# Optimization experiments

Hardware: AMD Instinct MI355X
Metric: run time of the kernel (lower is better)

## Reference

```python
import jax, jax.numpy as jnp
import numpy as np

N_VARS = 200000
M_CONS = 100000
NNZ = 1600000
HID = 128
NEG_SLOPE = 0.01  # torch F.leaky_relu default


def setup_inputs() -> dict:
    key = jax.random.key(0)
    ks = jax.random.split(key, 14)
    s = 0.05
    return {
        "primal": jax.random.normal(ks[0], (N_VARS, HID), jnp.float32),
        "last_primal": jax.random.normal(ks[1], (N_VARS, HID), jnp.float32),
        "dual": jax.random.normal(ks[2], (M_CONS, HID), jnp.float32),
        "rows": jax.random.randint(ks[3], (NNZ,), 0, M_CONS),
        "cols": jax.random.randint(ks[4], (NNZ,), 0, N_VARS),
        "vals": jax.random.normal(ks[5], (NNZ,), jnp.float32),
        "right_hand_side": jax.random.normal(ks[6], (M_CONS, HID), jnp.float32),
        "W1": jax.random.normal(ks[7], (HID, HID), jnp.float32) * s,
        "b1": jax.random.normal(ks[8], (HID,), jnp.float32) * s,
        "W2": jax.random.normal(ks[9], (HID, HID), jnp.float32) * s,
        "b2": jax.random.normal(ks[10], (HID,), jnp.float32) * s,
        "W3": jax.random.normal(ks[11], (HID, HID), jnp.float32) * s,
        "b3": jax.random.normal(ks[12], (HID,), jnp.float32) * s,
        "sigma": jnp.asarray(2.0, jnp.float32),
    }


def reference(primal, last_primal, dual, rows, cols, vals, right_hand_side,
              W1, b1, W2, b2, W3, b3, sigma):
    # X = Theta2(primal) - Theta3(last_primal): [n_vars, hid]
    X = (primal @ W2.T + b2) - (last_primal @ W3.T + b3)
    # sparse.mm(A_coo, X): gather source rows, scale by nnz vals, scatter-add to constraint rows
    msgs = vals[:, None] * X[cols]                      # [nnz, hid]
    AX = jax.ops.segment_sum(msgs, rows, num_segments=M_CONS)  # [m_cons, hid]
    pre = (dual @ W1.T + b1) + sigma * (AX - right_hand_side)
    return jnp.where(pre >= 0, pre, NEG_SLOPE * pre)
```

## Files before the change

kernel.cpp:

```cpp
#include <hip/hip_runtime.h>

#define HID 128
#define NEG_SLOPE 0.01f
#define NB 256
#define CHUNK 2048
#define MAX_RB 512
#define CAP 8192

typedef __attribute__((ext_vector_type(8))) short short8;
typedef __attribute__((ext_vector_type(4))) float f32x4;
typedef __attribute__((ext_vector_type(4))) unsigned u32x4;

__device__ inline unsigned short f2bfu(float f) {
    unsigned u = __float_as_uint(f);
    u += 0x7fff + ((u >> 16) & 1);
    return (unsigned short)(u >> 16);
}
__device__ inline float bf2f_lo(unsigned x) { return __uint_as_float((x & 0xffffu) << 16); }
__device__ inline float bf2f_hi(unsigned x) { return __uint_as_float(x & 0xffff0000u); }

__device__ inline unsigned cvtpk(float lo, float hi) {
    unsigned r;
    asm("v_cvt_pk_bf16_f32 %0, %1, %2" : "=v"(r) : "v"(lo), "v"(hi));
    return r;
}

#define MFMA_SW(accv, wfrag, xfrag) \
    asm("v_mfma_f32_16x16x32_bf16 %0, %1, %2, %0" : "+v"(accv) : "v"(wfrag), "v"(xfrag))

__global__ __launch_bounds__(256) void k_prep(
    const float* __restrict__ W1, const float* __restrict__ W2, const float* __restrict__ W3,
    unsigned short* __restrict__ Wcat, short8* __restrict__ W1F)
{
    int gid = blockIdx.x * 256 + threadIdx.x;
    if (gid < 128 * 256) {
        int n = gid >> 8, k = gid & 255;
        float v = (k < 128) ? W2[n * 128 + k] : -W3[n * 128 + (k - 128)];
        Wcat[gid] = f2bfu(v);
    } else if (gid < 128 * 256 + 2048) {
        int e = gid - 128 * 256;
        int lane = e & 63, ks = (e >> 6) & 3, nb = e >> 8;
        int row = nb * 16 + (lane & 15);
        int k0 = ks * 32 + ((lane >> 4) << 3);
        short8 v;
        #pragma unroll
        for (int j = 0; j < 8; ++j)
            v[j] = (short)f2bfu(W1[row * 128 + k0 + j]);
        W1F[e] = v;
    }
}

__device__ inline void load_a(const float* __restrict__ Ap, long rowbase, int nrows_tot,
                              int rrow, int rcol, float4 (&araw)[2][8])
{
    const float4 z4 = {0.f, 0.f, 0.f, 0.f};
    #pragma unroll
    for (int rg = 0; rg < 2; ++rg) {
        long row = rowbase + rrow + rg * 16;
        const float4* rp = (const float4*)(Ap + row * HID + rcol);
        if (row < nrows_tot) {
            #pragma unroll
            for (int ks = 0; ks < 4; ++ks) {
                araw[rg][ks * 2 + 0] = rp[ks * 8 + 0];
                araw[rg][ks * 2 + 1] = rp[ks * 8 + 1];
            }
        } else {
            #pragma unroll
            for (int u = 0; u < 8; ++u) araw[rg][u] = z4;
        }
    }
}

__device__ inline void conv_a(const float4 (&araw)[2][8], u32x4 (&af)[2][4])
{
    #pragma unroll
    for (int rg = 0; rg < 2; ++rg)
        #pragma unroll
        for (int ks = 0; ks < 4; ++ks) {
            float4 x0 = araw[rg][ks * 2 + 0], x1 = araw[rg][ks * 2 + 1];
            af[rg][ks][0] = cvtpk(x0.x, x0.y);
            af[rg][ks][1] = cvtpk(x0.z, x0.w);
            af[rg][ks][2] = cvtpk(x1.x, x1.y);
            af[rg][ks][3] = cvtpk(x1.z, x1.w);
        }
}

__device__ inline void mfma_half(f32x4 (&acc)[2][8], const u32x4 (&af)[2][4],
                                 const short8* Blds, int base, int l)
{
    #pragma unroll
    for (int ks = 0; ks < 4; ++ks)
        #pragma unroll
        for (int nb = 0; nb < 8; ++nb) {
            short8 bv = Blds[base + (nb * 4 + ks) * 64 + l];
            MFMA_SW(acc[0][nb], bv, af[0][ks]);
            MFMA_SW(acc[1][nb], bv, af[1][ks]);
        }
}

__global__ __launch_bounds__(256, 2) void k_theta_bfill(
    const float* __restrict__ primal, const float* __restrict__ lastp,
    const short8* __restrict__ Wcat,
    const float* __restrict__ b2, const float* __restrict__ b3,
    unsigned short* __restrict__ Xb, int nvars, int ntiles, int tgrid,
    const int* __restrict__ rows, const int* __restrict__ cols, const float* __restrict__ vals,
    int* __restrict__ cursor, int2* __restrict__ tmp_rc, float* __restrict__ tmp_v, int nnz, int rb,
    const float* __restrict__ dual, const short8* __restrict__ W1F,
    const float* __restrict__ b1, const float* __restrict__ rhs,
    const float* __restrict__ sigp, float* __restrict__ predual, int mcons, int nchunks)
{
    __shared__ short8 Blds[4096];
    const int t = threadIdx.x;

    if (blockIdx.x < (unsigned)tgrid) {
        const int l = t & 63, wv = t >> 6;
        const int rrow = wv * 32 + (l & 15);
        const int rcol = (l >> 4) << 3;
        const int colb = (l >> 4) << 2;

        float4 araw[2][8];
        const long tile0 = blockIdx.x;
        load_a(primal, tile0 * 128, nvars, rrow, rcol, araw);

        #pragma unroll
        for (int i = 0; i < 16; ++i) {
            int e = t + i * 256;
            int lane = e & 63, ks = (e >> 6) & 3, nb = (e >> 8) & 7, hf = e >> 11;
            int row = nb * 16 + (lane & 15);
            int col8 = (hf * 128 + ks * 32 + ((lane >> 4) << 3)) >> 3;
            Blds[e] = Wcat[row * 32 + col8];
        }

        float4 bias[8];
        #pragma unroll
        for (int nb = 0; nb < 8; ++nb) {
            int col = nb * 16 + colb;
            float4 p = *(const float4*)&b2[col];
            float4 q = *(const float4*)&b3[col];
            bias[nb] = make_float4(p.x - q.x, p.y - q.y, p.z - q.z, p.w - q.w);
        }

        __syncthreads();

        const f32x4 z = {0.f, 0.f, 0.f, 0.f};
        f32x4 acc[2][8];
        #pragma unroll
        for (int rg = 0; rg < 2; ++rg)
            #pragma unroll
            for (int nb = 0; nb < 8; ++nb) acc[rg][nb] = z;

        u32x4 af[2][4];

        #pragma unroll 1
        for (long tile = tile0; tile < ntiles; tile += tgrid) {
            conv_a(araw, af);
            load_a(lastp, tile * 128, nvars, rrow, rcol, araw);
            mfma_half(acc, af, Blds, 0, l);

            conv_a(araw, af);
            long nt = tile + tgrid;
            if (nt < ntiles) load_a(primal, nt * 128, nvars, rrow, rcol, araw);
            mfma_half(acc, af, Blds, 2048, l);

            asm volatile("s_nop 7\ns_nop 7");
            #pragma unroll
            for (int rg = 0; rg < 2; ++rg) {
                long row = tile * 128 + rrow + rg * 16;
                if (row < nvars) {
                    #pragma unroll
                    for (int nb = 0; nb < 8; ++nb) {
                        uint2 w;
                        w.x = cvtpk(acc[rg][nb][0] + bias[nb].x, acc[rg][nb][1] + bias[nb].y);
                        w.y = cvtpk(acc[rg][nb][2] + bias[nb].z, acc[rg][nb][3] + bias[nb].w);
                        *(uint2*)&Xb[row * HID + nb * 16 + colb] = w;
                    }
                }
                #pragma unroll
                for (int nb = 0; nb < 8; ++nb) acc[rg][nb] = z;
            }
        }
    } else if (blockIdx.x < (unsigned)(tgrid + nchunks)) {
        int* hist  = (int*)Blds;
        int* basep = hist + NB;
        int cb = blockIdx.x - tgrid;
        long cbase = (long)cb * CHUNK;
        hist[t] = 0;
        __syncthreads();

        int r[8], c[8], b[8], loc[8];
        float v[8];
        #pragma unroll
        for (int i = 0; i < 8; ++i) {
            long e = cbase + i * 256 + t;
            int locv = -1; int bi = 0; int ri = 0, ci = 0; float vi = 0.f;
            if (e < nnz) {
                ri = rows[e]; ci = cols[e]; vi = vals[e];
                bi = ri / rb;
                locv = atomicAdd(&hist[bi], 1);
            }
            r[i] = ri; c[i] = ci; v[i] = vi; b[i] = bi; loc[i] = locv;
        }
        __syncthreads();
        if (hist[t] > 0) basep[t] = atomicAdd(&cursor[t], hist[t]);
        __syncthreads();
        #pragma unroll
        for (int i = 0; i < 8; ++i) {
            if (loc[i] >= 0) {
                int o = basep[b[i]] + loc[i];
                if (o < CAP) {
                    long slot = (long)b[i] * CAP + o;
                    tmp_rc[slot] = make_int2(r[i], c[i]);
                    tmp_v[slot]  = v[i];
                }
            }
        }
    } else {
        const int l = t & 63, wv = t >> 6;
        const int rrow = wv * 32 + (l & 15);
        const int rcol = (l >> 4) << 3;
        const int colb = (l >> 4) << 2;
        const float sigma = *sigp;
        const long rowbase = (long)(blockIdx.x - tgrid - nchunks) * 128;

        float4 araw[2][8];
        load_a(dual, rowbase, mcons, rrow, rcol, araw);

        u32x4 af[2][4];
        conv_a(araw, af);

        const f32x4 z = {0.f, 0.f, 0.f, 0.f};
        f32x4 acc[2][8];
        #pragma unroll
        for (int rg = 0; rg < 2; ++rg)
            #pragma unroll
            for (int nb = 0; nb < 8; ++nb) acc[rg][nb] = z;

        #pragma unroll
        for (int ks = 0; ks < 4; ++ks)
            #pragma unroll
            for (int nb = 0; nb < 8; ++nb) {
                short8 bv = W1F[(nb * 4 + ks) * 64 + l];
                MFMA_SW(acc[0][nb], bv, af[0][ks]);
                MFMA_SW(acc[1][nb], bv, af[1][ks]);
            }
        asm volatile("s_nop 7\ns_nop 7");

        float4 bias[8];
        #pragma unroll
        for (int nb = 0; nb < 8; ++nb)
            bias[nb] = *(const float4*)&b1[nb * 16 + colb];

        #pragma unroll
        for (int rg = 0; rg < 2; ++rg) {
            long row = rowbase + rrow + rg * 16;
            if (row < mcons) {
                #pragma unroll
                for (int nb = 0; nb < 8; ++nb) {
                    long idx = row * HID + nb * 16 + colb;
                    float4 r4 = *(const float4*)&rhs[idx];
                    float4 pre;
                    pre.x = acc[rg][nb][0] + bias[nb].x - sigma * r4.x;
                    pre.y = acc[rg][nb][1] + bias[nb].y - sigma * r4.y;
                    pre.z = acc[rg][nb][2] + bias[nb].z - sigma * r4.z;
                    pre.w = acc[rg][nb][3] + bias[nb].w - sigma * r4.w;
                    *(float4*)&predual[idx] = pre;
                }
            }
        }
    }
}

__global__ __launch_bounds__(256) void k_csr(
    const int2* __restrict__ tmp_rc, const float* __restrict__ tmp_v,
    const int* __restrict__ bucket_fill,
    int* __restrict__ rowstart, int* __restrict__ count, int2* __restrict__ pairs,
    int m, int rb)
{
    __shared__ int cnt[MAX_RB];
    __shared__ int cur[MAX_RB];
    int b = blockIdx.x, t = threadIdx.x;
    int row0 = b * rb;
    int nrows = m - row0; if (nrows > rb) nrows = rb;
    if (nrows <= 0) return;

    for (int i = t; i < nrows; i += 256) cnt[i] = 0;
    __syncthreads();

    long e0 = (long)b * CAP;
    int fill = bucket_fill[b]; if (fill > CAP) fill = CAP;
    long e1 = e0 + fill;
    for (long e = e0 + t; e < e1; e += 256)
        atomicAdd(&cnt[tmp_rc[e].x - row0], 1);
    __syncthreads();

    if (t == 0) {
        int run = (int)e0;
        for (int i = 0; i < nrows; ++i) { cur[i] = run; run += cnt[i]; }
    }
    __syncthreads();

    for (int i = t; i < nrows; i += 256) {
        rowstart[row0 + i] = cur[i];
        count[row0 + i]    = cnt[i];
    }
    __syncthreads();

    for (long e = e0 + t; e < e1; e += 256) {
        int2 rc = tmp_rc[e];
        float vv = tmp_v[e];
        int slot = atomicAdd(&cur[rc.x - row0], 1);
        pairs[slot] = make_int2(rc.y, __float_as_int(vv));
    }
}

__global__ __launch_bounds__(256) void k_segsum(
    const int2* __restrict__ pairs, const int* __restrict__ rowstart, const int* __restrict__ count,
    const unsigned short* __restrict__ Xb, const float* __restrict__ predual,
    const float* __restrict__ sigp, float* __restrict__ out, int m)
{
    int w = (blockIdx.x * 256 + threadIdx.x) >> 6;
    int lane = threadIdx.x & 63;
    int half = lane >> 5;
    int sub  = lane & 31;
    int row  = w * 2 + half;
    bool valid = row < m;
    int start = valid ? rowstart[row] : 0;
    int cnt   = valid ? count[row]    : 0;

    int c0 = __shfl(cnt, 0);
    int c1 = __shfl(cnt, 32);
    int cmax = (c0 > c1) ? c0 : c1;

    const unsigned short* xb = Xb + sub * 4;

    float a0 = 0.f, a1 = 0.f, a2 = 0.f, a3 = 0.f;
    for (int j = 0; j < cmax; j += 8) {
        int2 p[8]; uint2 x[8];
        #pragma unroll
        for (int u = 0; u < 8; ++u) {
            bool act = (j + u) < cnt;
            int2 pv = make_int2(0, 0);
            if (act) pv = pairs[start + j + u];
            p[u] = pv;
        }
        #pragma unroll
        for (int u = 0; u < 8; ++u)
            x[u] = *(const uint2*)(xb + (size_t)p[u].x * HID);
        #pragma unroll
        for (int u = 0; u < 8; ++u) {
            float v = __int_as_float(p[u].y);
            a0 += v * bf2f_lo(x[u].x);
            a1 += v * bf2f_hi(x[u].x);
            a2 += v * bf2f_lo(x[u].y);
            a3 += v * bf2f_hi(x[u].y);
        }
    }
    if (valid) {
        float sg = *sigp;
        float4 pd = ((const float4*)predual)[(size_t)row * 32 + sub];
        float4 pre;
        pre.x = pd.x + sg * a0;
        pre.y = pd.y + sg * a1;
        pre.z = pd.z + sg * a2;
        pre.w = pd.w + sg * a3;
        pre.x = (pre.x >= 0.f) ? pre.x : NEG_SLOPE * pre.x;
        pre.y = (pre.y >= 0.f) ? pre.y : NEG_SLOPE * pre.y;
        pre.z = (pre.z >= 0.f) ? pre.z : NEG_SLOPE * pre.z;
        pre.w = (pre.w >= 0.f) ? pre.w : NEG_SLOPE * pre.w;
        ((float4*)out)[(size_t)row * 32 + sub] = pre;
    }
}

extern "C" void kernel_launch(void* const* d_in, const int* in_sizes, int n_in,
                              void* d_out, int out_size, void* d_ws, size_t ws_size,
                              hipStream_t stream) {
    const float* primal = (const float*)d_in[0];
    const float* lastp  = (const float*)d_in[1];
    const float* dual   = (const float*)d_in[2];
    const int*   rows   = (const int*)d_in[3];
    const int*   cols   = (const int*)d_in[4];
    const float* vals   = (const float*)d_in[5];
    const float* rhs    = (const float*)d_in[6];
    const float* W1     = (const float*)d_in[7];
    const float* b1     = (const float*)d_in[8];
    const float* W2     = (const float*)d_in[9];
    const float* b2     = (const float*)d_in[10];
    const float* W3     = (const float*)d_in[11];
    const float* b3     = (const float*)d_in[12];
    const float* sigp   = (const float*)d_in[13];

    const int nvars = in_sizes[0] / HID;
    const int mcons = in_sizes[2] / HID;
    const int nnz   = in_sizes[3];
    const int rb    = (mcons + NB - 1) / NB;

    float* out = (float*)d_out;

    char* wsb = (char*)d_ws;
    unsigned short* Xb = (unsigned short*)wsb;
    size_t off = (size_t)nvars * HID * sizeof(unsigned short);
    int2* pairs   = (int2*)(wsb + off);  off += (size_t)NB * CAP * sizeof(int2);
    int2* tmp_rc  = (int2*)(wsb + off);  off += (size_t)NB * CAP * sizeof(int2);
    float* tmp_v  = (float*)(wsb + off); off += (size_t)NB * CAP * sizeof(float);
    float* predual= (float*)(wsb + off); off += (size_t)mcons * HID * sizeof(float);
    unsigned short* Wcat = (unsigned short*)(wsb + off); off += 128 * 256 * 2;
    short8* W1F   = (short8*)(wsb + off); off += 2048 * sizeof(short8);
    int* count    = (int*)(wsb + off); off += (size_t)mcons * sizeof(int);
    int* rowstart = (int*)(wsb + off); off += (size_t)mcons * sizeof(int);
    int* cursor   = (int*)(wsb + off); off += NB * sizeof(int);

    hipMemsetAsync(cursor, 0, NB * sizeof(int), stream);

    k_prep<<<136, 256, 0, stream>>>(W1, W2, W3, Wcat, W1F);

    const int ntiles = (nvars + 127) / 128;
    const int tgrid = 512;
    const int nchunks = (nnz + CHUNK - 1) / CHUNK;
    const int pblocks = (mcons + 127) / 128;
    k_theta_bfill<<<tgrid + nchunks + pblocks, 256, 0, stream>>>(
        primal, lastp, (const short8*)Wcat, b2, b3, Xb, nvars, ntiles, tgrid,
        rows, cols, vals, cursor, tmp_rc, tmp_v, nnz, rb,
        dual, W1F, b1, rhs, sigp, predual, mcons, nchunks);

    k_csr<<<NB, 256, 0, stream>>>(tmp_rc, tmp_v, cursor,
                                  rowstart, count, pairs, mcons, rb);

    int nwaves = (mcons + 1) / 2;
    k_segsum<<<(nwaves + 3) / 4, 256, 0, stream>>>(
        pairs, rowstart, count, Xb, predual, sigp, out, mcons);
}
```

Before: 231.8 us.

## Store predual intermediate in bf16 and process four rows per wave in segsum

The dual-projection intermediate is now written as packed bf16 instead of fp32, which halves its write traffic and the segsum read traffic. The segsum kernel is remapped so each wave handles four rows, with each lane loading 16 bytes (8 bf16 features) per gathered X row rather than 8 bytes. This gives wider gathers and fewer waves, but adds more serialization when row counts differ within a wave and costs precision in the predual term.

```diff
diff --git a/kernel.cpp b/kernel.cpp
--- a/kernel.cpp
+++ b/kernel.cpp
@@ -107,7 +107,7 @@
     int* __restrict__ cursor, int2* __restrict__ tmp_rc, float* __restrict__ tmp_v, int nnz, int rb,
     const float* __restrict__ dual, const short8* __restrict__ W1F,
     const float* __restrict__ b1, const float* __restrict__ rhs,
-    const float* __restrict__ sigp, float* __restrict__ predual, int mcons, int nchunks)
+    const float* __restrict__ sigp, unsigned short* __restrict__ predualb, int mcons, int nchunks)
 {
     __shared__ short8 Blds[4096];
     const int t = threadIdx.x;
@@ -258,12 +258,12 @@
                 for (int nb = 0; nb < 8; ++nb) {
                     long idx = row * HID + nb * 16 + colb;
                     float4 r4 = *(const float4*)&rhs[idx];
-                    float4 pre;
-                    pre.x = acc[rg][nb][0] + bias[nb].x - sigma * r4.x;
-                    pre.y = acc[rg][nb][1] + bias[nb].y - sigma * r4.y;
-                    pre.z = acc[rg][nb][2] + bias[nb].z - sigma * r4.z;
-                    pre.w = acc[rg][nb][3] + bias[nb].w - sigma * r4.w;
-                    *(float4*)&predual[idx] = pre;
+                    uint2 w;
+                    w.x = cvtpk(acc[rg][nb][0] + bias[nb].x - sigma * r4.x,
+                                acc[rg][nb][1] + bias[nb].y - sigma * r4.y);
+                    w.y = cvtpk(acc[rg][nb][2] + bias[nb].z - sigma * r4.z,
+                                acc[rg][nb][3] + bias[nb].w - sigma * r4.w);
+                    *(uint2*)&predualb[idx] = w;
                 }
             }
         }
@@ -315,27 +315,30 @@
 
 __global__ __launch_bounds__(256) void k_segsum(
     const int2* __restrict__ pairs, const int* __restrict__ rowstart, const int* __restrict__ count,
-    const unsigned short* __restrict__ Xb, const float* __restrict__ predual,
+    const unsigned short* __restrict__ Xb, const unsigned short* __restrict__ predualb,
     const float* __restrict__ sigp, float* __restrict__ out, int m)
 {
     int w = (blockIdx.x * 256 + threadIdx.x) >> 6;
     int lane = threadIdx.x & 63;
-    int half = lane >> 5;
-    int sub  = lane & 31;
-    int row  = w * 2 + half;
+    int q = lane >> 4;
+    int sub = lane & 15;
+    int row = w * 4 + q;
     bool valid = row < m;
     int start = valid ? rowstart[row] : 0;
     int cnt   = valid ? count[row]    : 0;
 
     int c0 = __shfl(cnt, 0);
-    int c1 = __shfl(cnt, 32);
-    int cmax = (c0 > c1) ? c0 : c1;
-
-    const unsigned short* xb = Xb + sub * 4;
+    int c1 = __shfl(cnt, 16);
+    int c2 = __shfl(cnt, 32);
+    int c3 = __shfl(cnt, 48);
+    int cmax = max(max(c0, c1), max(c2, c3));
+
+    const unsigned short* xb = Xb + sub * 8;
 
     float a0 = 0.f, a1 = 0.f, a2 = 0.f, a3 = 0.f;
+    float a4 = 0.f, a5 = 0.f, a6 = 0.f, a7 = 0.f;
     for (int j = 0; j < cmax; j += 8) {
-        int2 p[8]; uint2 x[8];
+        int2 p[8]; u32x4 x[8];
         #pragma unroll
         for (int u = 0; u < 8; ++u) {
             bool act = (j + u) < cnt;
@@ -345,29 +348,39 @@
         }
         #pragma unroll
         for (int u = 0; u < 8; ++u)
-            x[u] = *(const uint2*)(xb + (size_t)p[u].x * HID);
+            x[u] = *(const u32x4*)(xb + (size_t)p[u].x * HID);
         #pragma unroll
         for (int u = 0; u < 8; ++u) {
             float v = __int_as_float(p[u].y);
-            a0 += v * bf2f_lo(x[u].x);
-            a1 += v * bf2f_hi(x[u].x);
-            a2 += v * bf2f_lo(x[u].y);
-            a3 += v * bf2f_hi(x[u].y);
+            a0 += v * bf2f_lo(x[u][0]); a1 += v * bf2f_hi(x[u][0]);
+            a2 += v * bf2f_lo(x[u][1]); a3 += v * bf2f_hi(x[u][1]);
+            a4 += v * bf2f_lo(x[u][2]); a5 += v * bf2f_hi(x[u][2]);
+            a6 += v * bf2f_lo(x[u][3]); a7 += v * bf2f_hi(x[u][3]);
         }
     }
     if (valid) {
         float sg = *sigp;
-        float4 pd = ((const float4*)predual)[(size_t)row * 32 + sub];
-        float4 pre;
-        pre.x = pd.x + sg * a0;
-        pre.y = pd.y + sg * a1;
-        pre.z = pd.z + sg * a2;
-        pre.w = pd.w + sg * a3;
-        pre.x = (pre.x >= 0.f) ? pre.x : NEG_SLOPE * pre.x;
-        pre.y = (pre.y >= 0.f) ? pre.y : NEG_SLOPE * pre.y;
-        pre.z = (pre.z >= 0.f) ? pre.z : NEG_SLOPE * pre.z;
-        pre.w = (pre.w >= 0.f) ? pre.w : NEG_SLOPE * pre.w;
-        ((float4*)out)[(size_t)row * 32 + sub] = pre;
+        long base = (size_t)row * HID + sub * 8;
+        u32x4 pd = *(const u32x4*)&predualb[base];
+        float4 o0, o1;
+        o0.x = bf2f_lo(pd[0]) + sg * a0;
+        o0.y = bf2f_hi(pd[0]) + sg * a1;
+        o0.z = bf2f_lo(pd[1]) + sg * a2;
+        o0.w = bf2f_hi(pd[1]) + sg * a3;
+        o1.x = bf2f_lo(pd[2]) + sg * a4;
+        o1.y = bf2f_hi(pd[2]) + sg * a5;
+        o1.z = bf2f_lo(pd[3]) + sg * a6;
+        o1.w = bf2f_hi(pd[3]) + sg * a7;
+        o0.x = (o0.x >= 0.f) ? o0.x : NEG_SLOPE * o0.x;
+        o0.y = (o0.y >= 0.f) ? o0.y : NEG_SLOPE * o0.y;
+        o0.z = (o0.z >= 0.f) ? o0.z : NEG_SLOPE * o0.z;
+        o0.w = (o0.w >= 0.f) ? o0.w : NEG_SLOPE * o0.w;
+        o1.x = (o1.x >= 0.f) ? o1.x : NEG_SLOPE * o1.x;
+        o1.y = (o1.y >= 0.f) ? o1.y : NEG_SLOPE * o1.y;
+        o1.z = (o1.z >= 0.f) ? o1.z : NEG_SLOPE * o1.z;
+        o1.w = (o1.w >= 0.f) ? o1.w : NEG_SLOPE * o1.w;
+        *(float4*)&out[base]     = o0;
+        *(float4*)&out[base + 4] = o1;
     }
 }
 
@@ -402,7 +415,8 @@
     int2* pairs   = (int2*)(wsb + off);  off += (size_t)NB * CAP * sizeof(int2);
     int2* tmp_rc  = (int2*)(wsb + off);  off += (size_t)NB * CAP * sizeof(int2);
     float* tmp_v  = (float*)(wsb + off); off += (size_t)NB * CAP * sizeof(float);
-    float* predual= (float*)(wsb + off); off += (size_t)mcons * HID * sizeof(float);
+    unsigned short* predualb = (unsigned short*)(wsb + off);
+    off += (size_t)mcons * HID * sizeof(unsigned short);
     unsigned short* Wcat = (unsigned short*)(wsb + off); off += 128 * 256 * 2;
     short8* W1F   = (short8*)(wsb + off); off += 2048 * sizeof(short8);
     int* count    = (int*)(wsb + off); off += (size_t)mcons * sizeof(int);
@@ -420,12 +434,12 @@
     k_theta_bfill<<<tgrid + nchunks + pblocks, 256, 0, stream>>>(
         primal, lastp, (const short8*)Wcat, b2, b3, Xb, nvars, ntiles, tgrid,
         rows, cols, vals, cursor, tmp_rc, tmp_v, nnz, rb,
-        dual, W1F, b1, rhs, sigp, predual, mcons, nchunks);
+        dual, W1F, b1, rhs, sigp, predualb, mcons, nchunks);
 
     k_csr<<<NB, 256, 0, stream>>>(tmp_rc, tmp_v, cursor,
                                   rowstart, count, pairs, mcons, rb);
 
-    int nwaves = (mcons + 1) / 2;
+    int nwaves = (mcons + 3) / 4;
     k_segsum<<<(nwaves + 3) / 4, 256, 0, stream>>>(
-        pairs, rowstart, count, Xb, predual, sigp, out, mcons);
-}
+        pairs, rowstart, count, Xb, predualb, sigp, out, mcons);
+}
```

Measured after the change: 218.8 us. 1.06x faster.
